# Kernel optimization log

Hardware: AMD Instinct MI355X
Metric: run time of the kernel (lower is better)

Reference implementation:

```python
import jax, jax.numpy as jnp
import numpy as np

WS, OWS, NH, C = 16, 24, 6, 192


def setup_inputs() -> dict:
    key = jax.random.key(0)
    ks = jax.random.split(key, 20)
    s = 0.05
    inp = {
        'x': jax.random.normal(ks[0], (2, C, 128, 128), jnp.float32),
        'depth': jax.random.normal(ks[1], (2, C, 128, 128), jnp.float32),
        'rpi': jax.random.randint(ks[2], (WS * WS, OWS * OWS), 0, (WS + OWS - 1) ** 2),
        'norm1_w': jnp.ones((C,), jnp.float32),
        'norm1_b': jnp.zeros((C,), jnp.float32),
        'qkv_w': jax.random.normal(ks[3], (C, 3 * C), jnp.float32) * s,
        'qkv_b': jax.random.normal(ks[4], (3 * C,), jnp.float32) * s,
        'dproj_w': jax.random.normal(ks[5], (C, C), jnp.float32) * s,
        'dproj_b': jax.random.normal(ks[6], (C,), jnp.float32) * s,
        'rpb_table': jax.random.normal(ks[7], ((WS + OWS - 1) ** 2, NH), jnp.float32) * 0.02,
        'proj_w': jax.random.normal(ks[8], (C, C), jnp.float32) * s,
        'proj_b': jax.random.normal(ks[9], (C,), jnp.float32) * s,
        'norm2_w': jnp.ones((C,), jnp.float32),
        'norm2_b': jnp.zeros((C,), jnp.float32),
        'fc1_w': jax.random.normal(ks[10], (C, 2 * C), jnp.float32) * s,
        'fc1_b': jax.random.normal(ks[11], (2 * C,), jnp.float32) * s,
        'fc2_w': jax.random.normal(ks[12], (2 * C, C), jnp.float32) * s,
        'fc2_b': jax.random.normal(ks[13], (C,), jnp.float32) * s,
    }
    return inp


def _ln(t, g, b):
    mu = t.mean(-1, keepdims=True)
    var = ((t - mu) ** 2).mean(-1, keepdims=True)
    return (t - mu) / jnp.sqrt(var + 1e-5) * g + b


def reference(x, depth, rpi, norm1_w, norm1_b, qkv_w, qkv_b, dproj_w, dproj_b,
              rpb_table, proj_w, proj_b, norm2_w, norm2_b, fc1_w, fc1_b, fc2_w, fc2_b):
    b, c, h, w = x.shape
    d = c // NH
    scale = d ** -0.5
    pad = (OWS - WS) // 2
    nh, nw = h // WS, w // WS

    xf = jnp.transpose(x, (0, 2, 3, 1))  # b h w c
    qkv = _ln(xf, norm1_w, norm1_b) @ qkv_w + qkv_b  # b h w 3c
    k, v = qkv[..., c:2 * c], qkv[..., 2 * c:]
    # depth_proj is a 1x1 conv == per-pixel linear
    q = jnp.einsum('bhwi,oi->bhwo', jnp.transpose(depth, (0, 2, 3, 1)), dproj_w) + dproj_b

    # non-overlapping query windows
    qw = q.reshape(b, nh, WS, nw, WS, c).transpose(0, 1, 3, 2, 4, 5).reshape(-1, WS * WS, c)

    # overlapping KV windows (unfold: kernel OWS, stride WS, pad (OWS-WS)//2)
    kv = jnp.concatenate([k, v], axis=-1)  # b h w 2c
    kvp = jnp.pad(kv, ((0, 0), (pad, pad), (pad, pad), (0, 0)))
    hh = (jnp.arange(nh) * WS)[:, None] + jnp.arange(OWS)[None]  # [nh, OWS]
    ww = (jnp.arange(nw) * WS)[:, None] + jnp.arange(OWS)[None]  # [nw, OWS]
    patches = kvp[:, hh[:, None, :, None], ww[None, :, None, :], :]  # b nh nw OWS OWS 2c
    patches = patches.reshape(-1, OWS * OWS, 2 * c)
    kw, vw = patches[..., :c], patches[..., c:]

    B, nq, n = qw.shape[0], WS * WS, OWS * OWS
    qh = qw.reshape(B, nq, NH, d).transpose(0, 2, 1, 3) * scale
    kh = kw.reshape(B, n, NH, d).transpose(0, 2, 1, 3)
    vh = vw.reshape(B, n, NH, d).transpose(0, 2, 1, 3)

    attn = jnp.einsum('bhqd,bhkd->bhqk', qh, kh)
    bias = rpb_table[rpi.reshape(-1)].reshape(nq, n, NH).transpose(2, 0, 1)  # H nq n
    attn = jax.nn.softmax(attn + bias[None], axis=-1)
    out = jnp.einsum('bhqk,bhkd->bhqd', attn, vh).transpose(0, 2, 1, 3).reshape(B, nq, c)

    out = out.reshape(b, nh, nw, WS, WS, c).transpose(0, 1, 3, 2, 4, 5).reshape(b, h, w, c)
    out = out @ proj_w + proj_b + xf  # residual
    y = out + (jax.nn.gelu(_ln(out, norm2_w, norm2_b) @ fc1_w + fc1_b, approximate=False) @ fc2_w + fc2_b)
    return jnp.transpose(y, (0, 3, 1, 2))
```

## Files before the change

### kernel.cpp

```cpp
#include <hip/hip_runtime.h>
#include <math.h>

typedef __attribute__((ext_vector_type(8))) short s16x8;
typedef __attribute__((ext_vector_type(4))) short s16x4;
typedef __attribute__((ext_vector_type(4))) float f32x4;

#define DEV __device__ __forceinline__

DEV float b2f(unsigned short u){ unsigned int x = ((unsigned int)u)<<16u; return __builtin_bit_cast(float,x); }
DEV unsigned short f2b(float f){
  unsigned int x = __builtin_bit_cast(unsigned int,f);
  x += 0x7fffu + ((x>>16)&1u);
  return (unsigned short)(x>>16);
}
DEV unsigned int pk_bf16(float lo, float hi){
  unsigned int r;
  asm("v_cvt_pk_bf16_f32 %0, %1, %2" : "=v"(r) : "v"(lo), "v"(hi));
  return r;
}
DEV float ex2(float x){
  float r;
  asm("v_exp_f32 %0, %1" : "=v"(r) : "v"(x));
  return r;
}
DEV float rcpf(float x){
  float r;
  asm("v_rcp_f32 %0, %1" : "=v"(r) : "v"(x));
  return r;
}
#define LOG2E 1.4426950408889634f

__global__ __launch_bounds__(256) void prep_all(
    const float* __restrict__ x, const float* __restrict__ depth,
    const float* __restrict__ g, const float* __restrict__ be,
    const float* __restrict__ qkvw, const float* __restrict__ dprojw,
    const float* __restrict__ projw, const float* __restrict__ fc1w,
    const float* __restrict__ fc2w, const int* __restrict__ rpi,
    const float* __restrict__ rpb,
    unsigned short* xn, unsigned short* xf, unsigned short* dn,
    unsigned short* kvw, unsigned short* dpw, unsigned short* pjw,
    unsigned short* f1w, unsigned short* f2w, unsigned short* bt){
  __shared__ float t[64][193];
  __shared__ float ps[4][64], pq[4][64];
  __shared__ float mu_s[64], rs_s[64];
  int tid = threadIdx.x;
  int bid = blockIdx.x;
  if(bid >= 512){
    int i = (bid - 512)*256 + tid;
    if(i < 73728){
      int n = i/192, k = i - n*192;
      kvw[i] = f2b(qkvw[k*576 + 192 + n]);
    } else if(i < 110592){
      int j = i - 73728;
      dpw[j] = f2b(dprojw[j]);
    } else if(i < 147456){
      int j = i - 110592; int n = j/192, k = j - n*192;
      pjw[j] = f2b(projw[k*192 + n]);
    } else if(i < 221184){
      int j = i - 147456; int n = j/192, k = j - n*192;
      f1w[j] = f2b(fc1w[k*384 + n]);
    } else if(i < 294912){
      int j = i - 221184; int n = j/384, k = j - n*384;
      f2w[j] = f2b(fc2w[k*192 + n]);
    } else {
      int j = i - 294912;
      int h = j/147456; int rr = j - h*147456;
      int kk = rr >> 8; int q = rr & 255;
      int step = kk >> 5, within = kk & 31;
      int lg = within >> 3, p4r = within & 7;
      bt[h*147456 + step*8192 + lg*2048 + q*8 + p4r] =
          f2b(rpb[rpi[q*576 + kk]*6 + h] * LOG2E);
    }
    return;
  }
  long tokbase = (long)bid * 64;
  int b = (int)(tokbase >> 14); int hw = (int)(tokbase & 16383);
  const float* xb = x + ((long)b*192)*16384 + hw;
  int tok = tid & 63, cpart = tid >> 6;
  for(int c = cpart; c < 192; c += 4) t[tok][c] = xb[(long)c*16384 + tok];
  __syncthreads();
  float s = 0.f, q = 0.f;
  #pragma unroll 4
  for(int i = 0; i < 48; i++){ float v = t[tok][cpart*48 + i]; s += v; q += v*v; }
  ps[cpart][tok] = s; pq[cpart][tok] = q;
  __syncthreads();
  if(tid < 64){
    float ss = ps[0][tid]+ps[1][tid]+ps[2][tid]+ps[3][tid];
    float qq = pq[0][tid]+pq[1][tid]+pq[2][tid]+pq[3][tid];
    float mu = ss * (1.f/192.f);
    float var = qq * (1.f/192.f) - mu*mu;
    mu_s[tid] = mu; rs_s[tid] = 1.f/sqrtf(var + 1e-5f);
  }
  __syncthreads();
  long obase = tokbase * 192;
  for(int u = tid; u < 64*192; u += 256){
    int tk = u / 192, ch = u - tk*192;
    float v = t[tk][ch];
    xf[obase + u] = f2b(v);
    xn[obase + u] = f2b((v - mu_s[tk]) * rs_s[tk] * g[ch] + be[ch]);
  }
  __syncthreads();
  const float* db = depth + ((long)b*192)*16384 + hw;
  for(int c = cpart; c < 192; c += 4) t[tok][c] = db[(long)c*16384 + tok];
  __syncthreads();
  for(int u = tid; u < 64*192; u += 256){
    int tk = u / 192, ch = u - tk*192;
    dn[obase + u] = f2b(t[tk][ch]);
  }
}

DEV void gemm_body(const unsigned short* __restrict__ A, const unsigned short* __restrict__ W,
                   const float* __restrict__ bias, const float* __restrict__ resf,
                   void* outp, int K, int N, int flags, int bid,
                   unsigned short* smem, int tid){
  unsigned short* Al = smem;
  unsigned short* Bl = smem + 9216;
  int lane = tid & 63, wv = tid >> 6;
  int wm = wv >> 1, wn = wv & 1, l15 = lane & 15, lg = lane >> 4;
  int X = bid & 7, j = bid >> 3;
  int mb = X + 8*(j & 31);
  int nb = j >> 5;
  long rowbase = (long)mb * 128;
  int colbase = nb * 64;
  f32x4 acc[4][2];
  #pragma unroll
  for(int m=0;m<4;m++)
    #pragma unroll
    for(int n=0;n<2;n++) acc[m][n] = (f32x4){0.f,0.f,0.f,0.f};
  int nk = K >> 6;
  for(int kt = 0; kt < nk; kt++){
    int k0 = kt*64;
    #pragma unroll
    for(int i = 0; i < 4; i++){
      int u = i*256 + tid; int r = u >> 3, c = u & 7;
      *(s16x8*)(Al + r*72 + c*8) = *(const s16x8*)(A + (rowbase + r)*(long)K + k0 + c*8);
    }
    #pragma unroll
    for(int i = 0; i < 2; i++){
      int u = i*256 + tid; int r = u >> 3, c = u & 7;
      *(s16x8*)(Bl + r*72 + c*8) = *(const s16x8*)(W + (long)(colbase + r)*K + k0 + c*8);
    }
    __syncthreads();
    #pragma unroll
    for(int kk = 0; kk < 64; kk += 32){
      s16x8 af[4], bf[2];
      #pragma unroll
      for(int m = 0; m < 4; m++) af[m] = *(const s16x8*)(Al + (wm*64 + m*16 + l15)*72 + kk + lg*8);
      #pragma unroll
      for(int n = 0; n < 2; n++) bf[n] = *(const s16x8*)(Bl + (wn*32 + n*16 + l15)*72 + kk + lg*8);
      #pragma unroll
      for(int m = 0; m < 4; m++)
        #pragma unroll
        for(int n = 0; n < 2; n++)
          acc[m][n] = __builtin_amdgcn_mfma_f32_16x16x32_bf16(af[m], bf[n], acc[m][n], 0, 0, 0);
    }
    __syncthreads();
  }
  if(flags & 8){
    float vloc[2][4][4];
    #pragma unroll
    for(int n = 0; n < 2; n++){
      int colg = colbase + wn*32 + n*16 + l15;
      float bs = bias[colg];
      #pragma unroll
      for(int m = 0; m < 4; m++){
        long rowg = rowbase + wm*64 + m*16 + lg*4;
        #pragma unroll
        for(int r = 0; r < 4; r++){
          long idx = (rowg + r)*(long)N + colg;
          vloc[n][m][r] = acc[m][n][r] + bs + resf[idx];
        }
      }
    }
    float* T = (float*)smem;
    #pragma unroll
    for(int n = 0; n < 2; n++){
      int chl = wn*32 + n*16 + l15;
      #pragma unroll
      for(int m = 0; m < 4; m++){
        int tl = wm*64 + m*16 + lg*4;
        #pragma unroll
        for(int r = 0; r < 4; r++) T[chl*132 + tl + r] = vloc[n][m][r];
      }
    }
    __syncthreads();
    int bb = (int)(rowbase >> 14), hw0 = (int)(rowbase & 16383);
    float* op = (float*)outp;
    for(int u = tid; u < 8192; u += 256){
      int chn = u >> 7, t2 = u & 127;
      op[((long)bb*192 + colbase + chn)*16384 + hw0 + t2] = T[chn*132 + t2];
    }
    return;
  }
  unsigned short* Ct = smem;
  #pragma unroll
  for(int n = 0; n < 2; n++){
    int colg_l = wn*32 + n*16 + l15;
    float bs = bias[colbase + colg_l];
    #pragma unroll
    for(int m = 0; m < 4; m++){
      int rowl = wm*64 + m*16 + lg*4;
      #pragma unroll
      for(int r = 0; r < 4; r++){
        float v = acc[m][n][r] + bs;
        if(flags & 1){
          float x2 = v*v;
          float u2 = -2.3021174f - 0.10294418f*x2;
          float sg = ex2(v*u2);
          v = v * rcpf(1.f + sg);
        }
        if(flags & 4) v *= (0.17677669529663687f * LOG2E);
        Ct[(rowl + r)*72 + colg_l] = f2b(v);
      }
    }
  }
  __syncthreads();
  unsigned short* op = (unsigned short*)outp;
  #pragma unroll
  for(int i = 0; i < 4; i++){
    int u = i*256 + tid;
    int tok = u >> 3, c8 = u & 7;
    *(s16x8*)(op + (rowbase + tok)*(long)N + colbase + c8*8) = *(const s16x8*)(Ct + tok*72 + c8*8);
  }
}

__global__ __launch_bounds__(256) void gemm_kvq(
    const unsigned short* __restrict__ xn, const unsigned short* __restrict__ dn,
    const unsigned short* __restrict__ kvw, const unsigned short* __restrict__ dpw,
    const float* __restrict__ kvb, const float* __restrict__ dpb,
    unsigned short* kv, unsigned short* qm){
  extern __shared__ unsigned short Bl[];
  int bid = blockIdx.x, tid = threadIdx.x;
  if(bid < 1536) gemm_body(xn, kvw, kvb, nullptr, kv, 192, 384, 0, bid, Bl, tid);
  else           gemm_body(dn, dpw, dpb, nullptr, qm, 192, 192, 4, bid - 1536, Bl, tid);
}

__global__ __launch_bounds__(256) void gemm2(
    const unsigned short* __restrict__ A, const unsigned short* __restrict__ W,
    const float* __restrict__ bias, const float* __restrict__ resf,
    void* outp, int K, int N, int flags){
  extern __shared__ unsigned short Bl[];
  gemm_body(A, W, bias, resf, outp, K, N, flags, blockIdx.x, Bl, threadIdx.x);
}

__global__ __launch_bounds__(512, 6) void attn_k(
    const unsigned short* __restrict__ qmat, const unsigned short* __restrict__ kvmat,
    const unsigned short* __restrict__ bt, unsigned short* __restrict__ omat){
  __shared__ unsigned short Kl[192*40];
  __shared__ unsigned short Vl[32*202];
  int tid = threadIdx.x, lane = tid & 63, wv = tid >> 6;
  int l15 = lane & 15, lg = lane >> 4;
  int bid = blockIdx.x;
  int X = bid & 7, j0 = bid >> 3;
  int win = X + 8*(j0 & 15);
  int h = j0 >> 4;
  int b = win >> 6, wi = (win >> 3) & 7, wj = win & 7;
  int qbase = wv*32;

  s16x8 qb[2];
  #pragma unroll
  for(int nt = 0; nt < 2; nt++){
    int q = qbase + nt*16 + l15;
    long tok = (long)b*16384 + (wi*16 + (q>>4))*128 + wj*16 + (q&15);
    qb[nt] = *(const s16x8*)(qmat + tok*192 + h*32 + lg*8);
  }
  const unsigned short* bq[2];
  #pragma unroll
  for(int nt = 0; nt < 2; nt++)
    bq[nt] = bt + h*147456 + lg*2048 + (qbase + nt*16 + l15)*8;

  float m_run[2] = {-1e30f, -1e30f};
  float l_run[2] = {0.f, 0.f};
  f32x4 oacc[2][2];
  #pragma unroll
  for(int mtd=0;mtd<2;mtd++)
    #pragma unroll
    for(int nt=0;nt<2;nt++) oacc[mtd][nt] = (f32x4){0.f,0.f,0.f,0.f};

  for(int ch = 0; ch < 3; ch++){
    __syncthreads();
    #pragma unroll
    for(int i = 0; i < 3; i++){
      int u = i*512 + tid;
      int p = u >> 3, w8 = u & 7;
      int isV = w8 >> 2, c = w8 & 3;
      int gp = ch*192 + p; int ii = gp / 24, jc = gp - ii*24;
      int gr = wi*16 - 4 + ii, gc = wj*16 - 4 + jc;
      bool ok = (gr >= 0) && (gr < 128) && (gc >= 0) && (gc < 128);
      s16x8 v = (s16x8){0,0,0,0,0,0,0,0};
      if(ok){
        long tok = (long)b*16384 + gr*128 + gc;
        v = *(const s16x8*)(kvmat + tok*384 + isV*192 + h*32 + c*8);
      }
      if(isV == 0){
        int pl = p & 31;
        int srow = (p & ~31) + ((pl & 4) << 2) + ((pl >> 3) << 2) + (pl & 3);
        *(s16x8*)(Kl + srow*40 + c*8) = v;
      } else {
        #pragma unroll
        for(int j2 = 0; j2 < 8; j2++) Vl[(c*8 + j2)*202 + p] = (unsigned short)v[j2];
      }
    }
    __syncthreads();
    #pragma unroll 1
    for(int kt = 0; kt < 6; kt++){
      int kb = kt*32;
      int step = ch*6 + kt;
      s16x8 ka[2];
      #pragma unroll
      for(int mt = 0; mt < 2; mt++) ka[mt] = *(const s16x8*)(Kl + (kb + mt*16 + l15)*40 + lg*8);
      f32x4 zf = (f32x4){0.f,0.f,0.f,0.f};
      f32x4 s[2][2];
      #pragma unroll
      for(int mt = 0; mt < 2; mt++)
        #pragma unroll
        for(int nt = 0; nt < 2; nt++)
          s[mt][nt] = __builtin_amdgcn_mfma_f32_16x16x32_bf16(ka[mt], qb[nt], zf, 0, 0, 0);
      #pragma unroll
      for(int nt = 0; nt < 2; nt++){
        s16x8 bv = *(const s16x8*)(bq[nt] + step*8192);
        #pragma unroll
        for(int mt = 0; mt < 2; mt++)
          #pragma unroll
          for(int r = 0; r < 4; r++) s[mt][nt][r] += b2f((unsigned short)bv[mt*4 + r]);
      }
      float lm[2];
      #pragma unroll
      for(int nt = 0; nt < 2; nt++){
        float v0 = fmaxf(fmaxf(s[0][nt][0], s[0][nt][1]), s[0][nt][2]);
        float v1 = fmaxf(fmaxf(s[0][nt][3], s[1][nt][0]), s[1][nt][1]);
        float v2 = fmaxf(fmaxf(s[1][nt][2], s[1][nt][3]), v0);
        float v = fmaxf(v1, v2);
        v = fmaxf(v, __shfl_xor(v, 16));
        v = fmaxf(v, __shfl_xor(v, 32));
        lm[nt] = v;
      }
      if(__any((lm[0] > m_run[0]) || (lm[1] > m_run[1]))){
        #pragma unroll
        for(int nt = 0; nt < 2; nt++){
          float nm = fmaxf(m_run[nt], lm[nt]);
          float fac = ex2(m_run[nt] - nm);
          m_run[nt] = nm;
          l_run[nt] *= fac;
          #pragma unroll
          for(int mtd = 0; mtd < 2; mtd++)
            #pragma unroll
            for(int r = 0; r < 4; r++) oacc[mtd][nt][r] *= fac;
        }
      }
      s16x8 pb[2];
      #pragma unroll
      for(int nt = 0; nt < 2; nt++){
        float p0 = ex2(s[0][nt][0] - m_run[nt]);
        float p1 = ex2(s[0][nt][1] - m_run[nt]);
        float p2 = ex2(s[0][nt][2] - m_run[nt]);
        float p3 = ex2(s[0][nt][3] - m_run[nt]);
        float p4 = ex2(s[1][nt][0] - m_run[nt]);
        float p5 = ex2(s[1][nt][1] - m_run[nt]);
        float p6 = ex2(s[1][nt][2] - m_run[nt]);
        float p7 = ex2(s[1][nt][3] - m_run[nt]);
        l_run[nt] += ((p0+p1)+(p2+p3)) + ((p4+p5)+(p6+p7));
        unsigned int w[4];
        w[0] = pk_bf16(p0, p1); w[1] = pk_bf16(p2, p3);
        w[2] = pk_bf16(p4, p5); w[3] = pk_bf16(p6, p7);
        pb[nt] = __builtin_bit_cast(s16x8, w);
      }
      s16x8 va[2];
      #pragma unroll
      for(int mtd = 0; mtd < 2; mtd++) va[mtd] = *(const s16x8*)(Vl + (mtd*16 + l15)*202 + kb + lg*8);
      #pragma unroll
      for(int mtd = 0; mtd < 2; mtd++)
        #pragma unroll
        for(int nt = 0; nt < 2; nt++)
          oacc[mtd][nt] = __builtin_amdgcn_mfma_f32_16x16x32_bf16(va[mtd], pb[nt], oacc[mtd][nt], 0, 0, 0);
    }
  }
  #pragma unroll
  for(int nt = 0; nt < 2; nt++){
    float l = l_run[nt];
    l += __shfl_xor(l, 16);
    l += __shfl_xor(l, 32);
    float inv = 1.f / l;
    int q = qbase + nt*16 + l15;
    long tok = (long)b*16384 + (wi*16 + (q>>4))*128 + wj*16 + (q&15);
    #pragma unroll
    for(int mtd = 0; mtd < 2; mtd++){
      s16x4 o;
      #pragma unroll
      for(int r = 0; r < 4; r++) o[r] = (short)f2b(oacc[mtd][nt][r] * inv);
      *(s16x4*)(omat + tok*192 + h*32 + mtd*16 + lg*4) = o;
    }
  }
}

__global__ __launch_bounds__(256) void proj_ln(
    const unsigned short* __restrict__ A, const unsigned short* __restrict__ W,
    const float* __restrict__ bias, const unsigned short* __restrict__ resb,
    const float* __restrict__ g2, const float* __restrict__ b2,
    float* __restrict__ r2, unsigned short* __restrict__ n2){
  extern __shared__ char smem[];
  unsigned short* Bl = (unsigned short*)smem;
  float* ps = (float*)(smem + 76800);
  float* pq = (float*)(smem + 77824);
  float* mu_s = (float*)(smem + 78848);
  float* rs_s = (float*)(smem + 79104);
  int tid = threadIdx.x, lane = tid & 63, wv = tid >> 6;
  int l15 = lane & 15, lg = lane >> 4;
  long rowbase = (long)blockIdx.x * 64;
  for(int u = tid; u < 192*24; u += 256){
    int row = u / 24, c = u - row*24;
    *(s16x8*)(Bl + row*200 + c*8) = *(const s16x8*)(W + row*192 + c*8);
  }
  __syncthreads();
  const unsigned short* ap[4];
  #pragma unroll
  for(int m = 0; m < 4; m++) ap[m] = A + (rowbase + m*16 + l15)*192 + lg*8;
  f32x4 acc[4][3];
  #pragma unroll
  for(int m=0;m<4;m++)
    #pragma unroll
    for(int n=0;n<3;n++) acc[m][n] = (f32x4){0.f,0.f,0.f,0.f};
  #pragma unroll 3
  for(int kk = 0; kk < 6; kk++){
    s16x8 af[4], bf[3];
    #pragma unroll
    for(int m = 0; m < 4; m++) af[m] = *(const s16x8*)(ap[m] + kk*32);
    #pragma unroll
    for(int n = 0; n < 3; n++) bf[n] = *(const s16x8*)(Bl + (wv*48 + n*16 + l15)*200 + kk*32 + lg*8);
    #pragma unroll
    for(int m = 0; m < 4; m++)
      #pragma unroll
      for(int n = 0; n < 3; n++)
        acc[m][n] = __builtin_amdgcn_mfma_f32_16x16x32_bf16(af[m], bf[n], acc[m][n], 0, 0, 0);
  }
  float val[4][3][4];
  float ts[4][4], tq[4][4];
  #pragma unroll
  for(int m=0;m<4;m++)
    #pragma unroll
    for(int r=0;r<4;r++){ ts[m][r]=0.f; tq[m][r]=0.f; }
  #pragma unroll
  for(int n = 0; n < 3; n++){
    int colg = wv*48 + n*16 + l15;
    float bs = bias[colg];
    #pragma unroll
    for(int m = 0; m < 4; m++){
      long rowg = rowbase + m*16 + lg*4;
      #pragma unroll
      for(int r = 0; r < 4; r++){
        long idx = (rowg + r)*192 + colg;
        float v = acc[m][n][r] + bs + b2f(resb[idx]);
        val[m][n][r] = v;
        ts[m][r] += v; tq[m][r] += v*v;
        r2[idx] = v;
      }
    }
  }
  #pragma unroll
  for(int m = 0; m < 4; m++)
    #pragma unroll
    for(int r = 0; r < 4; r++){
      float s1 = ts[m][r], q1 = tq[m][r];
      #pragma unroll
      for(int off = 1; off < 16; off <<= 1){
        s1 += __shfl_xor(s1, off);
        q1 += __shfl_xor(q1, off);
      }
      if(l15 == 0){
        int row = m*16 + lg*4 + r;
        ps[wv*64 + row] = s1; pq[wv*64 + row] = q1;
      }
    }
  __syncthreads();
  if(tid < 64){
    float ss = ps[tid] + ps[64+tid] + ps[128+tid] + ps[192+tid];
    float qq = pq[tid] + pq[64+tid] + pq[128+tid] + pq[192+tid];
    float mu = ss * (1.f/192.f);
    float var = qq * (1.f/192.f) - mu*mu;
    mu_s[tid] = mu; rs_s[tid] = 1.f/sqrtf(var + 1e-5f);
  }
  __syncthreads();
  #pragma unroll
  for(int n = 0; n < 3; n++){
    int colg = wv*48 + n*16 + l15;
    float gg = g2[colg], bb = b2[colg];
    #pragma unroll
    for(int m = 0; m < 4; m++){
      long rowg = rowbase + m*16 + lg*4;
      #pragma unroll
      for(int r = 0; r < 4; r++){
        int row = m*16 + lg*4 + r;
        long idx = (rowg + r)*192 + colg;
        n2[idx] = f2b((val[m][n][r] - mu_s[row]) * rs_s[row] * gg + bb);
      }
    }
  }
}

extern "C" void kernel_launch(void* const* d_in, const int* in_sizes, int n_in,
                              void* d_out, int out_size, void* d_ws, size_t ws_size,
                              hipStream_t stream) {
  const float* x     = (const float*)d_in[0];
  const float* depth = (const float*)d_in[1];
  const int*   rpi   = (const int*)d_in[2];
  const float* n1w   = (const float*)d_in[3];
  const float* n1b   = (const float*)d_in[4];
  const float* qkvw  = (const float*)d_in[5];
  const float* qkvb  = (const float*)d_in[6];
  const float* dprjw = (const float*)d_in[7];
  const float* dprjb = (const float*)d_in[8];
  const float* rpb   = (const float*)d_in[9];
  const float* prjw  = (const float*)d_in[10];
  const float* prjb  = (const float*)d_in[11];
  const float* n2w   = (const float*)d_in[12];
  const float* n2b   = (const float*)d_in[13];
  const float* fc1w  = (const float*)d_in[14];
  const float* fc1b  = (const float*)d_in[15];
  const float* fc2w  = (const float*)d_in[16];
  const float* fc2b  = (const float*)d_in[17];

  char* ws = (char*)d_ws;
  unsigned short* xn  = (unsigned short*)(ws + 0);
  unsigned short* dn  = (unsigned short*)(ws + 12582912);
  unsigned short* xf  = (unsigned short*)(ws + 25165824);
  unsigned short* kv  = (unsigned short*)(ws + 37748736);
  unsigned short* h1  = (unsigned short*)(ws + 37748736);
  unsigned short* qm  = (unsigned short*)(ws + 62914560);
  float*          r2  = (float*)(ws + 75497472);
  unsigned short* om  = (unsigned short*)(ws + 100663296);
  unsigned short* n2  = (unsigned short*)(ws + 100663296);
  unsigned short* kvw = (unsigned short*)(ws + 113246208);
  unsigned short* dpw = (unsigned short*)(ws + 113393664);
  unsigned short* pjw = (unsigned short*)(ws + 113467392);
  unsigned short* f1w = (unsigned short*)(ws + 113541120);
  unsigned short* f2w = (unsigned short*)(ws + 113688576);
  unsigned short* bt  = (unsigned short*)(ws + 113836032);

  prep_all<<<5120, 256, 0, stream>>>(x, depth, n1w, n1b, qkvw, dprjw, prjw, fc1w, fc2w,
                                     rpi, rpb, xn, xf, dn, kvw, dpw, pjw, f1w, f2w, bt);
  gemm_kvq<<<2304, 256, 27648, stream>>>(xn, dn, kvw, dpw, qkvb + 192, dprjb, kv, qm);
  attn_k<<<768, 512, 0, stream>>>(qm, kv, bt, om);
  proj_ln<<<512, 256, 79360, stream>>>(om, pjw, prjb, xf, n2w, n2b, r2, n2);
  gemm2<<<1536, 256, 27648, stream>>>(n2, f1w, fc1b, nullptr, h1, 192, 384, 1);
  gemm2<<<768, 256, 33792, stream>>>(h1, f2w, fc2b, r2, d_out, 384, 192, 8);
}
```

Baseline: 156.0 us.

## Split proj+LN2 kernel into generic GEMM with residual epilogue and separate LayerNorm

Replaces the fused proj_ln kernel, which used 64-row tiles with a large shared-memory weight copy, by the generic tiled GEMM path with a new epilogue that adds bias and the bf16 residual and writes fp32 through shared memory with vectorized stores. A separate lightweight LayerNorm kernel then reads the fp32 result and produces the bf16 normalized input for fc1. This aims at better GEMM efficiency and occupancy for the projection, at the cost of an extra kernel launch and an extra read of the fp32 intermediate.

```diff
diff --git a/kernel.cpp b/kernel.cpp
--- a/kernel.cpp
+++ b/kernel.cpp
@@ -110,8 +110,8 @@
 }
 
 DEV void gemm_body(const unsigned short* __restrict__ A, const unsigned short* __restrict__ W,
-                   const float* __restrict__ bias, const float* __restrict__ resf,
-                   void* outp, int K, int N, int flags, int bid,
+                   const float* __restrict__ bias, const unsigned short* __restrict__ resb,
+                   const float* __restrict__ resf, void* outp, int K, int N, int flags, int bid,
                    unsigned short* smem, int tid){
   unsigned short* Al = smem;
   unsigned short* Bl = smem + 9216;
@@ -192,6 +192,43 @@
     }
     return;
   }
+  if(flags & 2){
+    float vloc[2][4][4];
+    #pragma unroll
+    for(int n = 0; n < 2; n++){
+      int colg = colbase + wn*32 + n*16 + l15;
+      float bs = bias[colg];
+      #pragma unroll
+      for(int m = 0; m < 4; m++){
+        long rowg = rowbase + wm*64 + m*16 + lg*4;
+        #pragma unroll
+        for(int r = 0; r < 4; r++){
+          long idx = (rowg + r)*(long)N + colg;
+          vloc[n][m][r] = acc[m][n][r] + bs + b2f(resb[idx]);
+        }
+      }
+    }
+    float* T = (float*)smem;
+    #pragma unroll
+    for(int n = 0; n < 2; n++){
+      int colg_l = wn*32 + n*16 + l15;
+      #pragma unroll
+      for(int m = 0; m < 4; m++){
+        int rowl = wm*64 + m*16 + lg*4;
+        #pragma unroll
+        for(int r = 0; r < 4; r++) T[(rowl + r)*68 + colg_l] = vloc[n][m][r];
+      }
+    }
+    __syncthreads();
+    float* op = (float*)outp;
+    #pragma unroll
+    for(int i = 0; i < 8; i++){
+      int u = i*256 + tid;
+      int row = u >> 4, c4 = u & 15;
+      *(f32x4*)(op + (rowbase + row)*(long)N + colbase + c4*4) = *(const f32x4*)(T + row*68 + c4*4);
+    }
+    return;
+  }
   unsigned short* Ct = smem;
   #pragma unroll
   for(int n = 0; n < 2; n++){
@@ -231,16 +268,16 @@
     unsigned short* kv, unsigned short* qm){
   extern __shared__ unsigned short Bl[];
   int bid = blockIdx.x, tid = threadIdx.x;
-  if(bid < 1536) gemm_body(xn, kvw, kvb, nullptr, kv, 192, 384, 0, bid, Bl, tid);
-  else           gemm_body(dn, dpw, dpb, nullptr, qm, 192, 192, 4, bid - 1536, Bl, tid);
+  if(bid < 1536) gemm_body(xn, kvw, kvb, nullptr, nullptr, kv, 192, 384, 0, bid, Bl, tid);
+  else           gemm_body(dn, dpw, dpb, nullptr, nullptr, qm, 192, 192, 4, bid - 1536, Bl, tid);
 }
 
 __global__ __launch_bounds__(256) void gemm2(
     const unsigned short* __restrict__ A, const unsigned short* __restrict__ W,
-    const float* __restrict__ bias, const float* __restrict__ resf,
-    void* outp, int K, int N, int flags){
+    const float* __restrict__ bias, const unsigned short* __restrict__ resb,
+    const float* __restrict__ resf, void* outp, int K, int N, int flags){
   extern __shared__ unsigned short Bl[];
-  gemm_body(A, W, bias, resf, outp, K, N, flags, blockIdx.x, Bl, threadIdx.x);
+  gemm_body(A, W, bias, resb, resf, outp, K, N, flags, blockIdx.x, Bl, threadIdx.x);
 }
 
 __global__ __launch_bounds__(512, 6) void attn_k(
@@ -393,107 +430,41 @@
   }
 }
 
-__global__ __launch_bounds__(256) void proj_ln(
-    const unsigned short* __restrict__ A, const unsigned short* __restrict__ W,
-    const float* __restrict__ bias, const unsigned short* __restrict__ resb,
-    const float* __restrict__ g2, const float* __restrict__ b2,
-    float* __restrict__ r2, unsigned short* __restrict__ n2){
-  extern __shared__ char smem[];
-  unsigned short* Bl = (unsigned short*)smem;
-  float* ps = (float*)(smem + 76800);
-  float* pq = (float*)(smem + 77824);
-  float* mu_s = (float*)(smem + 78848);
-  float* rs_s = (float*)(smem + 79104);
-  int tid = threadIdx.x, lane = tid & 63, wv = tid >> 6;
-  int l15 = lane & 15, lg = lane >> 4;
-  long rowbase = (long)blockIdx.x * 64;
-  for(int u = tid; u < 192*24; u += 256){
-    int row = u / 24, c = u - row*24;
-    *(s16x8*)(Bl + row*200 + c*8) = *(const s16x8*)(W + row*192 + c*8);
-  }
-  __syncthreads();
-  const unsigned short* ap[4];
-  #pragma unroll
-  for(int m = 0; m < 4; m++) ap[m] = A + (rowbase + m*16 + l15)*192 + lg*8;
-  f32x4 acc[4][3];
-  #pragma unroll
-  for(int m=0;m<4;m++)
-    #pragma unroll
-    for(int n=0;n<3;n++) acc[m][n] = (f32x4){0.f,0.f,0.f,0.f};
-  #pragma unroll 3
-  for(int kk = 0; kk < 6; kk++){
-    s16x8 af[4], bf[3];
-    #pragma unroll
-    for(int m = 0; m < 4; m++) af[m] = *(const s16x8*)(ap[m] + kk*32);
-    #pragma unroll
-    for(int n = 0; n < 3; n++) bf[n] = *(const s16x8*)(Bl + (wv*48 + n*16 + l15)*200 + kk*32 + lg*8);
-    #pragma unroll
-    for(int m = 0; m < 4; m++)
-      #pragma unroll
-      for(int n = 0; n < 3; n++)
-        acc[m][n] = __builtin_amdgcn_mfma_f32_16x16x32_bf16(af[m], bf[n], acc[m][n], 0, 0, 0);
-  }
-  float val[4][3][4];
-  float ts[4][4], tq[4][4];
-  #pragma unroll
-  for(int m=0;m<4;m++)
-    #pragma unroll
-    for(int r=0;r<4;r++){ ts[m][r]=0.f; tq[m][r]=0.f; }
-  #pragma unroll
-  for(int n = 0; n < 3; n++){
-    int colg = wv*48 + n*16 + l15;
-    float bs = bias[colg];
-    #pragma unroll
-    for(int m = 0; m < 4; m++){
-      long rowg = rowbase + m*16 + lg*4;
-      #pragma unroll
-      for(int r = 0; r < 4; r++){
-        long idx = (rowg + r)*192 + colg;
-        float v = acc[m][n][r] + bs + b2f(resb[idx]);
-        val[m][n][r] = v;
-        ts[m][r] += v; tq[m][r] += v*v;
-        r2[idx] = v;
-      }
-    }
-  }
-  #pragma unroll
-  for(int m = 0; m < 4; m++)
-    #pragma unroll
-    for(int r = 0; r < 4; r++){
-      float s1 = ts[m][r], q1 = tq[m][r];
-      #pragma unroll
-      for(int off = 1; off < 16; off <<= 1){
-        s1 += __shfl_xor(s1, off);
-        q1 += __shfl_xor(q1, off);
-      }
-      if(l15 == 0){
-        int row = m*16 + lg*4 + r;
-        ps[wv*64 + row] = s1; pq[wv*64 + row] = q1;
-      }
-    }
-  __syncthreads();
-  if(tid < 64){
-    float ss = ps[tid] + ps[64+tid] + ps[128+tid] + ps[192+tid];
-    float qq = pq[tid] + pq[64+tid] + pq[128+tid] + pq[192+tid];
-    float mu = ss * (1.f/192.f);
-    float var = qq * (1.f/192.f) - mu*mu;
-    mu_s[tid] = mu; rs_s[tid] = 1.f/sqrtf(var + 1e-5f);
-  }
-  __syncthreads();
-  #pragma unroll
-  for(int n = 0; n < 3; n++){
-    int colg = wv*48 + n*16 + l15;
-    float gg = g2[colg], bb = b2[colg];
-    #pragma unroll
-    for(int m = 0; m < 4; m++){
-      long rowg = rowbase + m*16 + lg*4;
-      #pragma unroll
-      for(int r = 0; r < 4; r++){
-        int row = m*16 + lg*4 + r;
-        long idx = (rowg + r)*192 + colg;
-        n2[idx] = f2b((val[m][n][r] - mu_s[row]) * rs_s[row] * gg + bb);
-      }
-    }
+__global__ __launch_bounds__(256) void ln2_k(
+    const float* __restrict__ in, const float* __restrict__ g,
+    const float* __restrict__ be, unsigned short* __restrict__ out){
+  int tid = threadIdx.x;
+  long tok = (long)blockIdx.x*64 + (tid >> 2);
+  int cpart = tid & 3;
+  const float* ip = in + tok*192 + cpart*48;
+  f32x4 v[12];
+  float s = 0.f, q = 0.f;
+  #pragma unroll
+  for(int i = 0; i < 12; i++){
+    v[i] = *(const f32x4*)(ip + i*4);
+    #pragma unroll
+    for(int r = 0; r < 4; r++){ s += v[i][r]; q += v[i][r]*v[i][r]; }
+  }
+  s += __shfl_xor(s, 1); s += __shfl_xor(s, 2);
+  q += __shfl_xor(q, 1); q += __shfl_xor(q, 2);
+  float mu = s * (1.f/192.f);
+  float var = q * (1.f/192.f) - mu*mu;
+  float rs = 1.f/sqrtf(var + 1e-5f);
+  unsigned short* op = out + tok*192 + cpart*48;
+  const float* gp = g + cpart*48;
+  const float* bp = be + cpart*48;
+  #pragma unroll
+  for(int i = 0; i < 12; i++){
+    f32x4 g4 = *(const f32x4*)(gp + i*4);
+    f32x4 b4 = *(const f32x4*)(bp + i*4);
+    float o0 = (v[i][0] - mu)*rs*g4[0] + b4[0];
+    float o1 = (v[i][1] - mu)*rs*g4[1] + b4[1];
+    float o2 = (v[i][2] - mu)*rs*g4[2] + b4[2];
+    float o3 = (v[i][3] - mu)*rs*g4[3] + b4[3];
+    uint2 pk;
+    pk.x = pk_bf16(o0, o1);
+    pk.y = pk_bf16(o2, o3);
+    *(uint2*)(op + i*4) = pk;
   }
 }
 
@@ -540,7 +511,8 @@
                                      rpi, rpb, xn, xf, dn, kvw, dpw, pjw, f1w, f2w, bt);
   gemm_kvq<<<2304, 256, 27648, stream>>>(xn, dn, kvw, dpw, qkvb + 192, dprjb, kv, qm);
   attn_k<<<768, 512, 0, stream>>>(qm, kv, bt, om);
-  proj_ln<<<512, 256, 79360, stream>>>(om, pjw, prjb, xf, n2w, n2b, r2, n2);
-  gemm2<<<1536, 256, 27648, stream>>>(n2, f1w, fc1b, nullptr, h1, 192, 384, 1);
-  gemm2<<<768, 256, 33792, stream>>>(h1, f2w, fc2b, r2, d_out, 384, 192, 8);
-}
+  gemm2<<<768, 256, 34816, stream>>>(om, pjw, prjb, xf, nullptr, r2, 192, 192, 2);
+  ln2_k<<<512, 256, 0, stream>>>(r2, n2w, n2b, n2);
+  gemm2<<<1536, 256, 27648, stream>>>(n2, f1w, fc1b, nullptr, nullptr, h1, 192, 384, 1);
+  gemm2<<<768, 256, 33792, stream>>>(h1, f2w, fc2b, nullptr, r2, d_out, 384, 192, 8);
+}
```

Result: faster. 144.1 us (-7.7%).
